# Kernel optimization log

Hardware: AMD Instinct MI355X
Metric: run time of the kernel (lower is better)

Reference implementation:

```python
import jax, jax.numpy as jnp
import numpy as np

N = 131072      # total nodes in batch
D = 128         # input_dim
K_EXP = 1024    # input_dim * num_conv_kernels
H = 512         # cluster_model_hidden_dim
NG = 4          # number of groups (sub-models)
F_SEG = 8192    # fine clusters (global_max_pool segments)
G_SEG = 32      # coarse graphs (InstanceNorm segments)
C = 16          # node_num_classes
EPS = 1e-5      # InstanceNorm eps


def setup_inputs() -> dict:
    key = jax.random.key(0)
    ks = jax.random.split(key, 8)
    x = jax.random.normal(ks[0], (N, D), jnp.float32)
    # disjoint partition of node indices into NG groups (gather/scatter dispatch)
    group_indices = jax.random.permutation(ks[1], N).reshape(NG, N // NG)
    # sorted segment ids, every segment non-empty
    pool_cluster_fine = (jnp.arange(N) // (N // F_SEG)).astype(jnp.int32)
    batch_cluster_coarse = (jnp.arange(F_SEG) // (F_SEG // G_SEG)).astype(jnp.int32)
    # per-group NodeModel params: expand D -> K_EXP, relu, project -> H
    W1 = jax.random.normal(ks[2], (NG, D, K_EXP), jnp.float32) * (1.0 / np.sqrt(D))
    b1 = jnp.zeros((NG, K_EXP), jnp.float32)
    W2 = jax.random.normal(ks[3], (NG, K_EXP, H), jnp.float32) * (1.0 / np.sqrt(K_EXP))
    b2 = jnp.zeros((NG, H), jnp.float32)
    # classifier (glorot weight, zero bias)
    w_out = jax.random.normal(ks[4], (H, C), jnp.float32) * np.sqrt(2.0 / (H + C))
    b_out = jnp.zeros((C,), jnp.float32)
    return {"x": x, "group_indices": group_indices,
            "pool_cluster_fine": pool_cluster_fine,
            "batch_cluster_coarse": batch_cluster_coarse,
            "W1": W1, "b1": b1, "W2": W2, "b2": b2,
            "w_out": w_out, "b_out": b_out}


def reference(x, group_indices, pool_cluster_fine, batch_cluster_coarse,
              W1, b1, W2, b2, w_out, b_out):
    # per-group gather -> sub-model -> scatter (vectorized over groups)
    xg = x[group_indices]                                   # [NG, N/NG, D]
    h = jax.nn.relu(jnp.einsum('gnd,gdk->gnk', xg, W1) + b1[:, None, :])
    og = jnp.einsum('gnk,gkh->gnh', h, W2) + b2[:, None, :]  # [NG, N/NG, H]
    new_feat = jnp.zeros((x.shape[0], H), x.dtype).at[group_indices.reshape(-1)].set(
        og.reshape(-1, H))                                   # [N, H]
    # global_max_pool over fine clusters
    emb = jax.ops.segment_max(new_feat, pool_cluster_fine,
                              num_segments=F_SEG, indices_are_sorted=True)  # [F, H]
    # PyG InstanceNorm(affine=False): per coarse-graph, per-channel standardization
    ones = jnp.ones((F_SEG, 1), emb.dtype)
    cnt = jax.ops.segment_sum(ones, batch_cluster_coarse,
                              num_segments=G_SEG, indices_are_sorted=True)  # [G,1]
    mean = jax.ops.segment_sum(emb, batch_cluster_coarse,
                               num_segments=G_SEG, indices_are_sorted=True) / cnt
    var = jax.ops.segment_sum(emb * emb, batch_cluster_coarse,
                              num_segments=G_SEG, indices_are_sorted=True) / cnt - mean ** 2
    normed = (emb - mean[batch_cluster_coarse]) * jax.lax.rsqrt(var[batch_cluster_coarse] + EPS)
    # dropout is identity in eval mode; classifier
    logits = normed @ w_out + b_out                          # [F, C]
    return logits
```

## Files before the change

### kernel.cpp

```cpp
#include <hip/hip_runtime.h>
#include <stdint.h>

typedef __bf16 bf16;
typedef bf16 bf16x4 __attribute__((ext_vector_type(4)));
typedef bf16 bf16x8 __attribute__((ext_vector_type(8)));
typedef float f32x4 __attribute__((ext_vector_type(4)));

#define N_NODES 131072
#define D_IN    128
#define KEXP    1024
#define H_DIM   512
#define NGRP    4
#define NPG     32768
#define F_SEG   8192
#define G_SEG   32
#define C_OUT   16

typedef const __attribute__((address_space(1))) void* gas_t;
typedef __attribute__((address_space(3))) void* las_t;
__device__ __forceinline__ void cp16_async(const bf16* g, bf16* l) {
    __builtin_amdgcn_global_load_lds((gas_t)g, (las_t)l, 16, 0, 0);
}

__global__ void convert_weights(const float* __restrict__ W1,
                                const float* __restrict__ W2,
                                bf16* __restrict__ W1F,
                                bf16* __restrict__ W2F)
{
    int t = blockIdx.x * 256 + threadIdx.x;
    if (t < 65536) {
        int slot = t & 63, f = (t >> 6) & 7, kc = (t >> 9) & 31, g = t >> 14;
        int ks = f >> 1, kt = f & 1, quad = slot >> 4, ln = slot & 15;
        int k = kc * 32 + kt * 16 + ln;
        const float* src = W1 + ((size_t)(g * 128 + ks * 32 + quad * 8)) * 1024 + k;
        bf16x8 v;
        #pragma unroll
        for (int j = 0; j < 8; ++j) v[j] = (bf16)src[(size_t)j * 1024];
        *(bf16x8*)(W1F + (size_t)t * 8) = v;
    } else {
        int u = t - 65536;
        if (u < 262144) {
            int slot = u & 63, f = (u >> 6) & 15, kc = (u >> 10) & 31;
            int n0t2 = (u >> 15) & 1, g = u >> 16;
            int quad = slot >> 4, ln = slot & 15;
            int k = kc * 32 + quad * 8;
            int n = n0t2 * 256 + f * 16 + ln;
            const float* src = W2 + ((size_t)(g * 1024 + k)) * 512 + n;
            bf16x8 v;
            #pragma unroll
            for (int j = 0; j < 8; ++j) v[j] = (bf16)src[(size_t)j * 512];
            *(bf16x8*)(W2F + (size_t)u * 8) = v;
        }
    }
}

__global__ __launch_bounds__(256, 3)
void mlp_kernel(const float* __restrict__ x,
                const int*   __restrict__ gidx,
                const bf16*  __restrict__ W1F,
                const float* __restrict__ b1,
                const bf16*  __restrict__ W2F,
                const float* __restrict__ b2,
                bf16*        __restrict__ NF)
{
    __shared__ __align__(16) bf16 sW1[2][4096];
    __shared__ __align__(16) bf16 sH[2][2048];
    __shared__ __align__(16) float sB1[1024];

    const int tid  = threadIdx.x;
    const int bid  = blockIdx.x;
    const int g    = bid >> 10;
    const int rem  = bid & 1023;
    const int m0   = (rem >> 1) * 64;
    const int n0t2 = rem & 1;

    const int wave = tid >> 6;
    const int lane = tid & 63;
    const int quad = lane >> 4;
    const int ln   = lane & 15;
    const int mg   = wave >> 1;
    const int ng   = wave & 1;

    const int*  gI  = gidx + g * NPG + m0;
    const bf16* W1g = W1F + (size_t)g * 131072;
    const bf16* W2g = W2F + (size_t)(g * 2 + n0t2) * 262144;

    bf16x8 xf[4];
    #pragma unroll
    for (int ks = 0; ks < 4; ++ks) {
        int row  = wave * 16 + ln;
        int node = gI[row];
        const float* src = x + (size_t)node * D_IN + ks * 32 + quad * 8;
        float4 a = *(const float4*)src;
        float4 b = *(const float4*)(src + 4);
        bf16x8 v;
        v[0] = (bf16)a.x; v[1] = (bf16)a.y; v[2] = (bf16)a.z; v[3] = (bf16)a.w;
        v[4] = (bf16)b.x; v[5] = (bf16)b.y; v[6] = (bf16)b.z; v[7] = (bf16)b.w;
        xf[ks] = v;
    }

    *(float4*)(sB1 + tid * 4) = *(const float4*)(b1 + g * KEXP + tid * 4);

    f32x4 acc2[2][8];
    #pragma unroll
    for (int a = 0; a < 2; ++a)
        #pragma unroll
        for (int b = 0; b < 8; ++b)
            acc2[a][b] = (f32x4){0.f, 0.f, 0.f, 0.f};

    auto do_stage1 = [&](int j) {
        const bf16* w1buf = sW1[j & 1];
        bf16*       hdst  = sH[j & 1];
        f32x4 acc1[2];
        acc1[0] = (f32x4){0.f, 0.f, 0.f, 0.f};
        acc1[1] = (f32x4){0.f, 0.f, 0.f, 0.f};
        #pragma unroll
        for (int ks = 0; ks < 4; ++ks) {
            #pragma unroll
            for (int kt = 0; kt < 2; ++kt) {
                bf16x8 w1f = *(const bf16x8*)(w1buf + ((ks * 2 + kt) * 64 + lane) * 8);
                acc1[kt] = __builtin_amdgcn_mfma_f32_16x16x32_bf16(
                    w1f, xf[ks], acc1[kt], 0, 0, 0);
            }
        }
        #pragma unroll
        for (int kt = 0; kt < 2; ++kt) {
            float4 bv = *(const float4*)(sB1 + j * 32 + kt * 16 + quad * 4);
            float bvr[4] = {bv.x, bv.y, bv.z, bv.w};
            int qa = kt * 2 + (quad >> 1);
            int j0 = (quad & 1) * 4;
            bf16x4 pk;
            #pragma unroll
            for (int reg = 0; reg < 4; ++reg)
                pk[reg] = (bf16)fmaxf(acc1[kt][reg] + bvr[reg], 0.f);
            *(bf16x4*)(hdst + (wave * 64 + qa * 16 + ln) * 8 + j0) = pk;
        }
    };

    __syncthreads();

    #pragma unroll
    for (int r = 0; r < 2; ++r) {
        int c = r * 4 + wave;
        cp16_async(W1g + c * 512 + lane * 8, sW1[0] + c * 512);
    }
    #pragma unroll
    for (int r = 0; r < 2; ++r) {
        int c = r * 4 + wave;
        cp16_async(W1g + 4096 + c * 512 + lane * 8, sW1[1] + c * 512);
    }
    asm volatile("s_waitcnt vmcnt(2)" ::: "memory");
    __builtin_amdgcn_s_barrier();

    do_stage1(0);

    #pragma unroll 1
    for (int j = 1; j < 32; ++j) {
        __syncthreads();

        bf16x8 bb[8];
        {
            const bf16* w2src = W2g + (size_t)(j - 1) * 8192 + ng * 4096;
            #pragma unroll
            for (int nt = 0; nt < 8; ++nt)
                bb[nt] = *(const bf16x8*)(w2src + nt * 512 + lane * 8);
        }

        {
            int nkc = (j + 1) & 31;
            const bf16* w1src = W1g + (size_t)nkc * 4096;
            bf16* d1 = sW1[(j + 1) & 1];
            #pragma unroll
            for (int r = 0; r < 2; ++r) {
                int c = r * 4 + wave;
                cp16_async(w1src + c * 512 + lane * 8, d1 + c * 512);
            }
        }

        __builtin_amdgcn_s_setprio(1);
        do_stage1(j);

        {
            const bf16* hbuf = sH[(j - 1) & 1];
            #pragma unroll
            for (int mt = 0; mt < 2; ++mt) {
                bf16x8 a2 = *(const bf16x8*)(hbuf + ((mg * 2 + mt) * 64 + lane) * 8);
                #pragma unroll
                for (int nt = 0; nt < 8; ++nt)
                    acc2[mt][nt] = __builtin_amdgcn_mfma_f32_16x16x32_bf16(
                        a2, bb[nt], acc2[mt][nt], 0, 0, 0);
            }
        }
        __builtin_amdgcn_s_setprio(0);
    }

    __syncthreads();
    {
        bf16x8 bb[8];
        const bf16* w2src = W2g + (size_t)31 * 8192 + ng * 4096;
        #pragma unroll
        for (int nt = 0; nt < 8; ++nt)
            bb[nt] = *(const bf16x8*)(w2src + nt * 512 + lane * 8);
        const bf16* hbuf = sH[1];
        #pragma unroll
        for (int mt = 0; mt < 2; ++mt) {
            bf16x8 a2 = *(const bf16x8*)(hbuf + ((mg * 2 + mt) * 64 + lane) * 8);
            #pragma unroll
            for (int nt = 0; nt < 8; ++nt)
                acc2[mt][nt] = __builtin_amdgcn_mfma_f32_16x16x32_bf16(
                    a2, bb[nt], acc2[mt][nt], 0, 0, 0);
        }
    }

    const float* b2g = b2 + g * H_DIM + n0t2 * 256 + ng * 128;
    float b2v[8];
    #pragma unroll
    for (int nt = 0; nt < 8; ++nt) b2v[nt] = b2g[nt * 16 + ln];

    #pragma unroll
    for (int mt = 0; mt < 2; ++mt)
        #pragma unroll
        for (int reg = 0; reg < 4; ++reg) {
            int row  = mg * 32 + mt * 16 + quad * 4 + reg;
            int node = gI[row];
            bf16* dst = NF + (size_t)node * H_DIM + n0t2 * 256 + ng * 128;
            #pragma unroll
            for (int nt = 0; nt < 8; ++nt)
                dst[nt * 16 + ln] = (bf16)(acc2[mt][nt][reg] + b2v[nt]);
        }
}

__global__ void pool_kernel(const bf16* __restrict__ NF, float* __restrict__ EMB)
{
    int t  = blockIdx.x * 256 + threadIdx.x;
    int f  = t >> 6;
    int c8 = (t & 63) * 8;
    const uint4* src = (const uint4*)(NF + (size_t)f * 16 * 512 + c8);
    float m[8];
    #pragma unroll
    for (int i = 0; i < 8; ++i) m[i] = -INFINITY;
    #pragma unroll
    for (int r = 0; r < 16; ++r) {
        uint4 v = src[(size_t)r * 64];
        uint32_t w[4] = {v.x, v.y, v.z, v.w};
        #pragma unroll
        for (int i = 0; i < 4; ++i) {
            m[2*i]   = fmaxf(m[2*i],   __uint_as_float(w[i] << 16));
            m[2*i+1] = fmaxf(m[2*i+1], __uint_as_float(w[i] & 0xffff0000u));
        }
    }
    float* dst = EMB + (size_t)f * 512 + c8;
    *(float4*)dst       = make_float4(m[0], m[1], m[2], m[3]);
    *(float4*)(dst + 4) = make_float4(m[4], m[5], m[6], m[7]);
}

__global__ void stats_kernel(const float* __restrict__ EMB,
                             float* __restrict__ MEAN,
                             float* __restrict__ RSIG)
{
    int gc = blockIdx.x;
    int ch = blockIdx.y * 128 + threadIdx.x;
    const float* p = EMB + (size_t)gc * 256 * 512 + ch;
    float s = 0.f, ss = 0.f;
    #pragma unroll 4
    for (int r = 0; r < 256; ++r) {
        float v = p[(size_t)r * 512];
        s += v; ss += v * v;
    }
    float mean = s * (1.f / 256.f);
    float var  = ss * (1.f / 256.f) - mean * mean;
    MEAN[gc * 512 + ch] = mean;
    RSIG[gc * 512 + ch] = rsqrtf(var + 1e-5f);
}

__global__ __launch_bounds__(256)
void classifier_kernel(const float* __restrict__ EMB,
                       const float* __restrict__ MEAN,
                       const float* __restrict__ RSIG,
                       const float* __restrict__ w_out,
                       const float* __restrict__ b_out,
                       float* __restrict__ out)
{
    __shared__ float sW[512 * 16];
    __shared__ float sE[16 * 513];
    int t  = threadIdx.x;
    int f0 = blockIdx.x * 16;
    int gc = f0 >> 8;

    #pragma unroll
    for (int it = 0; it < 8; ++it) {
        int i = (it * 256 + t) * 4;
        *(float4*)(sW + i) = *(const float4*)(w_out + i);
    }
    #pragma unroll
    for (int it = 0; it < 32; ++it) {
        int i  = it * 256 + t;
        int fr = i >> 9;
        int h  = i & 511;
        float v = EMB[(size_t)(f0 + fr) * 512 + h];
        sE[fr * 513 + h] = (v - MEAN[gc * 512 + h]) * RSIG[gc * 512 + h];
    }
    __syncthreads();

    int fr = t >> 4;
    int c  = t & 15;
    float acc = b_out[c];
    #pragma unroll 8
    for (int h = 0; h < 512; ++h)
        acc += sE[fr * 513 + h] * sW[h * 16 + c];
    out[(size_t)(f0 + fr) * 16 + c] = acc;
}

extern "C" void kernel_launch(void* const* d_in, const int* in_sizes, int n_in,
                              void* d_out, int out_size, void* d_ws, size_t ws_size,
                              hipStream_t stream)
{
    const float* x     = (const float*)d_in[0];
    const int*   gidx  = (const int*)d_in[1];
    const float* W1    = (const float*)d_in[4];
    const float* b1    = (const float*)d_in[5];
    const float* W2    = (const float*)d_in[6];
    const float* b2    = (const float*)d_in[7];
    const float* w_out = (const float*)d_in[8];
    const float* b_out = (const float*)d_in[9];
    float* out = (float*)d_out;

    char* w = (char*)d_ws;
    bf16* W1F = (bf16*)w;  w += (size_t)NGRP * KEXP * D_IN * 2;
    bf16* W2F = (bf16*)w;  w += (size_t)NGRP * H_DIM * KEXP * 2;
    bf16* NF  = (bf16*)w;  w += (size_t)N_NODES * H_DIM * 2;
    float* EMB  = (float*)w; w += (size_t)F_SEG * H_DIM * 4;
    float* MEAN = (float*)w; w += (size_t)G_SEG * H_DIM * 4;
    float* RSIG = (float*)w; w += (size_t)G_SEG * H_DIM * 4;

    convert_weights<<<1280, 256, 0, stream>>>(W1, W2, W1F, W2F);
    mlp_kernel<<<4096, 256, 0, stream>>>(x, gidx, W1F, b1, W2F, b2, NF);
    pool_kernel<<<2048, 256, 0, stream>>>(NF, EMB);
    stats_kernel<<<dim3(32, 4), 128, 0, stream>>>(EMB, MEAN, RSIG);
    classifier_kernel<<<512, 256, 0, stream>>>(EMB, MEAN, RSIG, w_out, b_out, out);
}
```

Measured before the change: 392.6 us.

## Make each wave own 16 rows and drop block-wide LDS staging and barriers

Reworks the fused MLP kernel so each wave handles its own 16 rows across all 256 output columns. Stage-1 weights are now read straight from global memory into registers instead of being staged asynchronously through shared memory, and the hidden activations go through a small per-wave LDS scratch. This removes the per-iteration __syncthreads and cross-wave dependencies. The cost is more registers (16 accumulators), lower occupancy (launch bounds 3 to 2), and more global/L2 traffic, since every wave reloads the full W1 and W2 tiles instead of sharing them.

```diff
diff --git a/kernel.cpp b/kernel.cpp
--- a/kernel.cpp
+++ b/kernel.cpp
@@ -15,12 +15,6 @@
 #define F_SEG   8192
 #define G_SEG   32
 #define C_OUT   16
-
-typedef const __attribute__((address_space(1))) void* gas_t;
-typedef __attribute__((address_space(3))) void* las_t;
-__device__ __forceinline__ void cp16_async(const bf16* g, bf16* l) {
-    __builtin_amdgcn_global_load_lds((gas_t)g, (las_t)l, 16, 0, 0);
-}
 
 __global__ void convert_weights(const float* __restrict__ W1,
                                 const float* __restrict__ W2,
@@ -54,7 +48,7 @@
     }
 }
 
-__global__ __launch_bounds__(256, 3)
+__global__ __launch_bounds__(256, 2)
 void mlp_kernel(const float* __restrict__ x,
                 const int*   __restrict__ gidx,
                 const bf16*  __restrict__ W1F,
@@ -63,8 +57,7 @@
                 const float* __restrict__ b2,
                 bf16*        __restrict__ NF)
 {
-    __shared__ __align__(16) bf16 sW1[2][4096];
-    __shared__ __align__(16) bf16 sH[2][2048];
+    __shared__ __align__(16) bf16 sT[4][512];
     __shared__ __align__(16) float sB1[1024];
 
     const int tid  = threadIdx.x;
@@ -78,18 +71,16 @@
     const int lane = tid & 63;
     const int quad = lane >> 4;
     const int ln   = lane & 15;
-    const int mg   = wave >> 1;
-    const int ng   = wave & 1;
-
-    const int*  gI  = gidx + g * NPG + m0;
+
+    const int*  gI  = gidx + g * NPG + m0 + wave * 16;
     const bf16* W1g = W1F + (size_t)g * 131072;
     const bf16* W2g = W2F + (size_t)(g * 2 + n0t2) * 262144;
+    bf16* myT = sT[wave];
 
     bf16x8 xf[4];
     #pragma unroll
     for (int ks = 0; ks < 4; ++ks) {
-        int row  = wave * 16 + ln;
-        int node = gI[row];
+        int node = gI[ln];
         const float* src = x + (size_t)node * D_IN + ks * 32 + quad * 8;
         float4 a = *(const float4*)src;
         float4 b = *(const float4*)(src + 4);
@@ -100,29 +91,27 @@
     }
 
     *(float4*)(sB1 + tid * 4) = *(const float4*)(b1 + g * KEXP + tid * 4);
-
-    f32x4 acc2[2][8];
-    #pragma unroll
-    for (int a = 0; a < 2; ++a)
-        #pragma unroll
-        for (int b = 0; b < 8; ++b)
-            acc2[a][b] = (f32x4){0.f, 0.f, 0.f, 0.f};
-
-    auto do_stage1 = [&](int j) {
-        const bf16* w1buf = sW1[j & 1];
-        bf16*       hdst  = sH[j & 1];
+    __syncthreads();
+
+    f32x4 acc2[16];
+    #pragma unroll
+    for (int b = 0; b < 16; ++b) acc2[b] = (f32x4){0.f, 0.f, 0.f, 0.f};
+
+    auto do_stage1 = [&](int j) -> bf16x8 {
+        const bf16* w1 = W1g + (size_t)j * 4096;
+        bf16x8 w1f[8];
+        #pragma unroll
+        for (int f = 0; f < 8; ++f)
+            w1f[f] = *(const bf16x8*)(w1 + f * 512 + lane * 8);
         f32x4 acc1[2];
         acc1[0] = (f32x4){0.f, 0.f, 0.f, 0.f};
         acc1[1] = (f32x4){0.f, 0.f, 0.f, 0.f};
         #pragma unroll
-        for (int ks = 0; ks < 4; ++ks) {
+        for (int ks = 0; ks < 4; ++ks)
             #pragma unroll
-            for (int kt = 0; kt < 2; ++kt) {
-                bf16x8 w1f = *(const bf16x8*)(w1buf + ((ks * 2 + kt) * 64 + lane) * 8);
+            for (int kt = 0; kt < 2; ++kt)
                 acc1[kt] = __builtin_amdgcn_mfma_f32_16x16x32_bf16(
-                    w1f, xf[ks], acc1[kt], 0, 0, 0);
-            }
-        }
+                    w1f[ks * 2 + kt], xf[ks], acc1[kt], 0, 0, 0);
         #pragma unroll
         for (int kt = 0; kt < 2; ++kt) {
             float4 bv = *(const float4*)(sB1 + j * 32 + kt * 16 + quad * 4);
@@ -133,101 +122,66 @@
             #pragma unroll
             for (int reg = 0; reg < 4; ++reg)
                 pk[reg] = (bf16)fmaxf(acc1[kt][reg] + bvr[reg], 0.f);
-            *(bf16x4*)(hdst + (wave * 64 + qa * 16 + ln) * 8 + j0) = pk;
-        }
+            *(bf16x4*)(myT + (qa * 16 + ln) * 8 + j0) = pk;
+        }
+        return *(const bf16x8*)(myT + lane * 8);
     };
 
-    __syncthreads();
-
-    #pragma unroll
-    for (int r = 0; r < 2; ++r) {
-        int c = r * 4 + wave;
-        cp16_async(W1g + c * 512 + lane * 8, sW1[0] + c * 512);
-    }
-    #pragma unroll
-    for (int r = 0; r < 2; ++r) {
-        int c = r * 4 + wave;
-        cp16_async(W1g + 4096 + c * 512 + lane * 8, sW1[1] + c * 512);
-    }
-    asm volatile("s_waitcnt vmcnt(2)" ::: "memory");
-    __builtin_amdgcn_s_barrier();
-
-    do_stage1(0);
+    bf16x8 afp = do_stage1(0);
 
     #pragma unroll 1
     for (int j = 1; j < 32; ++j) {
-        __syncthreads();
-
-        bf16x8 bb[8];
-        {
-            const bf16* w2src = W2g + (size_t)(j - 1) * 8192 + ng * 4096;
-            #pragma unroll
-            for (int nt = 0; nt < 8; ++nt)
-                bb[nt] = *(const bf16x8*)(w2src + nt * 512 + lane * 8);
-        }
-
-        {
-            int nkc = (j + 1) & 31;
-            const bf16* w1src = W1g + (size_t)nkc * 4096;
-            bf16* d1 = sW1[(j + 1) & 1];
-            #pragma unroll
-            for (int r = 0; r < 2; ++r) {
-                int c = r * 4 + wave;
-                cp16_async(w1src + c * 512 + lane * 8, d1 + c * 512);
-            }
-        }
-
-        __builtin_amdgcn_s_setprio(1);
-        do_stage1(j);
-
-        {
-            const bf16* hbuf = sH[(j - 1) & 1];
-            #pragma unroll
-            for (int mt = 0; mt < 2; ++mt) {
-                bf16x8 a2 = *(const bf16x8*)(hbuf + ((mg * 2 + mt) * 64 + lane) * 8);
-                #pragma unroll
-                for (int nt = 0; nt < 8; ++nt)
-                    acc2[mt][nt] = __builtin_amdgcn_mfma_f32_16x16x32_bf16(
-                        a2, bb[nt], acc2[mt][nt], 0, 0, 0);
-            }
-        }
-        __builtin_amdgcn_s_setprio(0);
-    }
-
-    __syncthreads();
+        const bf16* w2 = W2g + (size_t)(j - 1) * 8192;
+
+        bf16x8 bb0[8];
+        #pragma unroll
+        for (int nt = 0; nt < 8; ++nt)
+            bb0[nt] = *(const bf16x8*)(w2 + nt * 512 + lane * 8);
+
+        bf16x8 afn = do_stage1(j);
+
+        #pragma unroll
+        for (int nt = 0; nt < 8; ++nt)
+            acc2[nt] = __builtin_amdgcn_mfma_f32_16x16x32_bf16(
+                afp, bb0[nt], acc2[nt], 0, 0, 0);
+
+        bf16x8 bb1[8];
+        #pragma unroll
+        for (int nt = 0; nt < 8; ++nt)
+            bb1[nt] = *(const bf16x8*)(w2 + (8 + nt) * 512 + lane * 8);
+
+        #pragma unroll
+        for (int nt = 0; nt < 8; ++nt)
+            acc2[8 + nt] = __builtin_amdgcn_mfma_f32_16x16x32_bf16(
+                afp, bb1[nt], acc2[8 + nt], 0, 0, 0);
+
+        afp = afn;
+    }
+
     {
-        bf16x8 bb[8];
-        const bf16* w2src = W2g + (size_t)31 * 8192 + ng * 4096;
-        #pragma unroll
-        for (int nt = 0; nt < 8; ++nt)
-            bb[nt] = *(const bf16x8*)(w2src + nt * 512 + lane * 8);
-        const bf16* hbuf = sH[1];
-        #pragma unroll
-        for (int mt = 0; mt < 2; ++mt) {
-            bf16x8 a2 = *(const bf16x8*)(hbuf + ((mg * 2 + mt) * 64 + lane) * 8);
-            #pragma unroll
-            for (int nt = 0; nt < 8; ++nt)
-                acc2[mt][nt] = __builtin_amdgcn_mfma_f32_16x16x32_bf16(
-                    a2, bb[nt], acc2[mt][nt], 0, 0, 0);
-        }
-    }
-
-    const float* b2g = b2 + g * H_DIM + n0t2 * 256 + ng * 128;
-    float b2v[8];
-    #pragma unroll
-    for (int nt = 0; nt < 8; ++nt) b2v[nt] = b2g[nt * 16 + ln];
-
-    #pragma unroll
-    for (int mt = 0; mt < 2; ++mt)
-        #pragma unroll
-        for (int reg = 0; reg < 4; ++reg) {
-            int row  = mg * 32 + mt * 16 + quad * 4 + reg;
-            int node = gI[row];
-            bf16* dst = NF + (size_t)node * H_DIM + n0t2 * 256 + ng * 128;
-            #pragma unroll
-            for (int nt = 0; nt < 8; ++nt)
-                dst[nt * 16 + ln] = (bf16)(acc2[mt][nt][reg] + b2v[nt]);
-        }
+        const bf16* w2 = W2g + (size_t)31 * 8192;
+        #pragma unroll
+        for (int nt = 0; nt < 16; ++nt) {
+            bf16x8 bb = *(const bf16x8*)(w2 + nt * 512 + lane * 8);
+            acc2[nt] = __builtin_amdgcn_mfma_f32_16x16x32_bf16(
+                afp, bb, acc2[nt], 0, 0, 0);
+        }
+    }
+
+    const float* b2g = b2 + g * H_DIM + n0t2 * 256;
+    float b2v[16];
+    #pragma unroll
+    for (int nt = 0; nt < 16; ++nt) b2v[nt] = b2g[nt * 16 + ln];
+
+    #pragma unroll
+    for (int reg = 0; reg < 4; ++reg) {
+        int row  = quad * 4 + reg;
+        int node = gI[row];
+        bf16* dst = NF + (size_t)node * H_DIM + n0t2 * 256;
+        #pragma unroll
+        for (int nt = 0; nt < 16; ++nt)
+            dst[nt * 16 + ln] = (bf16)(acc2[nt][reg] + b2v[nt]);
+    }
 }
 
 __global__ void pool_kernel(const bf16* __restrict__ NF, float* __restrict__ EMB)
```

New measurement: 554.2 us. +41.1%, slower.
